# Performance work log

Hardware: AMD Instinct MI355X
Metric: run time of the kernel (lower is better)

The kernel has to match this reference:

```python
import jax, jax.numpy as jnp
import numpy as np

BOS, PAD, EOS, UNK = 0, 1, 2, 3  # fairseq dictionary special-token ids
CHAR_VOCAB = 5000
DIM = 512
LATENT = 10000


def setup_inputs() -> dict:
    key = jax.random.key(0)
    k1, k2, k3 = jax.random.split(key, 3)
    # char-ngram ids per token: [B, T, max_char_len]
    x = jax.random.randint(k1, (8, 1024, 20), 0, CHAR_VOCAB, dtype=jnp.int64 if jax.config.jax_enable_x64 else jnp.int32)
    # char ngram embedding table (also serves as preset_emb for special tokens)
    char_table = jax.random.normal(k2, (CHAR_VOCAB, DIM), dtype=jnp.float32) * 0.05
    # fixed latent codebook, init std = latent**-0.5 as in the module
    latent_mat = jax.random.normal(k3, (LATENT, DIM), dtype=jnp.float32) * (LATENT ** -0.5)
    return {"x": x, "char_table": char_table, "latent_mat": latent_mat}


def reference(x, char_table, latent_mat):
    # --- CharacterNgramEmbedder: gather + sum-pool over char ngrams (pad masked) ---
    emb = char_table[x]                                   # [B, T, C, D]
    valid = (x != PAD)[..., None].astype(emb.dtype)       # pad ngrams contribute 0
    ngram_weight = jnp.sum(emb * valid, axis=2)           # [B, T, D]
    lang_emb = jnp.tanh(ngram_weight)

    # --- latent codebook attention: QK^T -> softmax -> V over fixed codebook ---
    latent_scores = jnp.einsum('btd,ld->btl', lang_emb, latent_mat)   # [B, T, L]
    latent_dist = jax.nn.softmax(latent_scores, axis=-1)
    latent_emb = jnp.einsum('btl,ld->btd', latent_dist, latent_mat)   # [B, T, D]
    sde_emb = lang_emb + latent_emb

    # --- preset_emb overwrite for special tokens (masked scatter) ---
    first = x[:, :, 0]                                    # [B, T]
    for tok in (PAD, BOS, EOS, UNK):
        sde_emb = jnp.where((first == tok)[..., None], char_table[tok], sde_emb)
    return sde_emb
```

## Files before the change

### kernel.cpp

```cpp
#include <hip/hip_runtime.h>

#define BT    8192
#define DIM   512
#define NLAT  10000
#define LPAD2 10240
#define NG    20

typedef short bf16x8 __attribute__((ext_vector_type(8)));
typedef float f32x4  __attribute__((ext_vector_type(4)));
typedef unsigned short u16;
typedef u16 u16x8 __attribute__((ext_vector_type(8)));
typedef u16 u16x4 __attribute__((ext_vector_type(4)));

static __device__ __forceinline__ u16 f2bf(float f) {
    union { float f; unsigned u; } v; v.f = f;
    unsigned r = v.u + 0x7FFF + ((v.u >> 16) & 1);
    return (u16)(r >> 16);
}

static __device__ __forceinline__ void gload16(const void* g, void* l) {
    __builtin_amdgcn_global_load_lds(
        (const __attribute__((address_space(1))) unsigned int*)g,
        (__attribute__((address_space(3))) unsigned int*)l,
        16, 0, 0);
}

__global__ __launch_bounds__(256) void lang_kernel(
        const int* __restrict__ x, const float* __restrict__ ct,
        float* __restrict__ lang, u16* __restrict__ qb) {
    const int tok = blockIdx.x * 2 + (threadIdx.x >> 7);
    const int tl  = threadIdx.x & 127;
    const int* xr = x + tok * NG;
    float4 s = make_float4(0.f, 0.f, 0.f, 0.f);
    #pragma unroll
    for (int j = 0; j < NG; ++j) {
        int c = xr[j];
        if (c != 1) {
            float4 v = *(const float4*)(ct + (long)c * DIM + tl * 4);
            s.x += v.x; s.y += v.y; s.z += v.z; s.w += v.w;
        }
    }
    float4 t = make_float4(tanhf(s.x), tanhf(s.y), tanhf(s.z), tanhf(s.w));
    *(float4*)(lang + (long)tok * DIM + tl * 4) = t;
    u16x4 o = { f2bf(t.x), f2bf(t.y), f2bf(t.z), f2bf(t.w) };
    *(u16x4*)(qb + (long)tok * DIM + tl * 4) = o;
}

__global__ __launch_bounds__(256) void conv_kernel(
        const float* __restrict__ lm, u16* __restrict__ kvg, u16* __restrict__ latT) {
    __shared__ u16 tile[64][514];
    const int lb = blockIdx.x * 64;
    const int t  = threadIdx.x;

    #pragma unroll 4
    for (int i = 0; i < 16; ++i) {
        int ch  = t + i * 256;
        int r   = ch >> 6;
        int c8  = ch & 63;
        int row = lb + r;
        u16x8 v = {0,0,0,0,0,0,0,0};
        if (row < NLAT) {
            const float* src = lm + (long)row * DIM + c8 * 8;
            float4 a = *(const float4*)src;
            float4 b = *(const float4*)(src + 4);
            v[0]=f2bf(a.x); v[1]=f2bf(a.y); v[2]=f2bf(a.z); v[3]=f2bf(a.w);
            v[4]=f2bf(b.x); v[5]=f2bf(b.y); v[6]=f2bf(b.z); v[7]=f2bf(b.w);
        }
        *(u16x8*)(kvg + (long)row * DIM + c8 * 8) = v;
        #pragma unroll
        for (int j = 0; j < 8; ++j) tile[r][c8 * 8 + j] = v[j];
    }
    __syncthreads();
    #pragma unroll 4
    for (int i = 0; i < 16; ++i) {
        int ch = t + i * 256;
        int d  = ch >> 3;
        int c8 = ch & 7;
        u16x8 v;
        #pragma unroll
        for (int j = 0; j < 8; ++j) v[j] = tile[c8 * 8 + j][d];
        *(u16x8*)(latT + (long)d * LPAD2 + lb + c8 * 8) = v;
    }
}

#define G_COMPUTE(buf) {                                                       \
    _Pragma("unroll")                                                          \
    for (int kc_ = 0; kc_ < 2; ++kc_) {                                        \
        const int xs_ = ((kc_ * 4 + g) ^ (lr & 7)) * 8;                        \
        bf16x8 af_[2], bf_[4];                                                 \
        _Pragma("unroll")                                                      \
        for (int mf_ = 0; mf_ < 2; ++mf_)                                      \
            af_[mf_] = *(const bf16x8*)&lds[buf][(wm * 32 + mf_ * 16 + lr) * 64 + xs_]; \
        _Pragma("unroll")                                                      \
        for (int nf_ = 0; nf_ < 4; ++nf_)                                      \
            bf_[nf_] = *(const bf16x8*)&lds[buf][8192 + (wn * 64 + nf_ * 16 + lr) * 64 + xs_]; \
        __builtin_amdgcn_s_setprio(1);                                         \
        _Pragma("unroll")                                                      \
        for (int mf_ = 0; mf_ < 2; ++mf_)                                      \
            _Pragma("unroll")                                                  \
            for (int nf_ = 0; nf_ < 4; ++nf_)                                  \
                acc[mf_][nf_] = __builtin_amdgcn_mfma_f32_16x16x32_bf16(       \
                    af_[mf_], bf_[nf_], acc[mf_][nf_], 0, 0, 0);               \
        __builtin_amdgcn_s_setprio(0);                                         \
    }                                                                          \
}

#define G1_STAGE(buf, kt) {                                                    \
    const int k0_ = (kt) * 64;                                                 \
    _Pragma("unroll")                                                          \
    for (int i_ = 0; i_ < 2; ++i_) {                                           \
        int ch_ = t + i_ * 512;                                                \
        int row_ = ch_ >> 3;                                                   \
        int sc_ = ((ch_ & 7) ^ (row_ & 7)) * 8;                                \
        gload16(Q + (m0 + row_) * (long)DIM + k0_ + sc_, &lds[buf][ch_ * 8]);  \
        gload16(Bgp + (long)row_ * DIM + k0_ + sc_, &lds[buf][8192 + ch_ * 8]);\
    }                                                                          \
}

__global__ __launch_bounds__(512, 4) void gemm1_kernel(
        const u16* __restrict__ Q, const u16* __restrict__ L,
        u16* __restrict__ P, float* __restrict__ rowsum,
        int n0_global, int npanels, int pstride) {
    __shared__ u16 lds[2][16384];

    const int nwg = 64 * npanels;
    const int cpx = nwg >> 3;
    const int bid = blockIdx.x;
    const int wg  = (bid & 7) * cpx + (bid >> 3);
    const int mb  = wg & 63;
    const int nb  = wg >> 6;
    const long m0    = (long)mb * 128;
    const int  ncol0 = n0_global + nb * 128;

    const u16* Bgp = L + (long)ncol0 * DIM;

    const int t = threadIdx.x, lane = t & 63, w = t >> 6;
    const int wm = w >> 1, wn = w & 1;
    const int g = lane >> 4, lr = lane & 15;

    f32x4 acc[2][4];
    #pragma unroll
    for (int m = 0; m < 2; ++m)
        #pragma unroll
        for (int n = 0; n < 4; ++n) acc[m][n] = f32x4{0.f,0.f,0.f,0.f};

    G1_STAGE(0, 0);
    G1_STAGE(1, 1);

    #pragma unroll 1
    for (int kt = 0; kt < 7; ++kt) {
        asm volatile("s_waitcnt vmcnt(4)" ::: "memory");
        __builtin_amdgcn_s_barrier();
        G_COMPUTE(kt & 1);
        __builtin_amdgcn_s_barrier();
        if (kt + 2 < 8) G1_STAGE(kt & 1, kt + 2);
    }
    asm volatile("s_waitcnt vmcnt(0)" ::: "memory");
    __builtin_amdgcn_s_barrier();
    G_COMPUTE(1);

    #pragma unroll
    for (int mf = 0; mf < 2; ++mf)
        #pragma unroll
        for (int nf = 0; nf < 4; ++nf) {
            const int col = ncol0 + wn * 64 + nf * 16 + lr;
            const bool ok = (col < NLAT);
            #pragma unroll
            for (int r = 0; r < 4; ++r)
                acc[mf][nf][r] = ok ? __expf(acc[mf][nf][r]) : 0.f;
        }

    #pragma unroll
    for (int mf = 0; mf < 2; ++mf) {
        float sv[4] = {0.f, 0.f, 0.f, 0.f};
        #pragma unroll
        for (int nf = 0; nf < 4; ++nf)
            #pragma unroll
            for (int r = 0; r < 4; ++r) sv[r] += acc[mf][nf][r];
        #pragma unroll
        for (int r = 0; r < 4; ++r) {
            float s = sv[r];
            s += __shfl_xor(s, 1); s += __shfl_xor(s, 2);
            s += __shfl_xor(s, 4); s += __shfl_xor(s, 8);
            if (lr == 0)
                atomicAdd(&rowsum[m0 + wm * 32 + mf * 16 + g * 4 + r], s);
        }
    }

    const int pcol0 = (ncol0 - n0_global) + wn * 64;
    #pragma unroll
    for (int mf = 0; mf < 2; ++mf)
        #pragma unroll
        for (int nf = 0; nf < 4; ++nf) {
            const int pc = pcol0 + nf * 16 + lr;
            #pragma unroll
            for (int r = 0; r < 4; ++r) {
                const long row = m0 + wm * 32 + mf * 16 + g * 4 + r;
                __builtin_nontemporal_store(f2bf(acc[mf][nf][r]),
                                            &P[row * (long)pstride + pc]);
            }
        }
}

#define G2_STAGE(buf, kt) {                                                    \
    const int kloc_ = (step_off + (kt)) * 64;                                  \
    _Pragma("unroll")                                                          \
    for (int i_ = 0; i_ < 2; ++i_) {                                           \
        int ch_ = t + i_ * 512;                                                \
        int row_ = ch_ >> 3;                                                   \
        int sc_ = ((ch_ & 7) ^ (row_ & 7)) * 8;                                \
        gload16(P + (m0 + row_) * (long)pstride + kloc_ + sc_, &lds[buf][ch_ * 8]); \
        gload16(LT + (long)(nbase + row_) * LPAD2 + n0_global + kloc_ + sc_,   \
                &lds[buf][8192 + ch_ * 8]);                                    \
    }                                                                          \
}

__global__ __launch_bounds__(512, 4) void gemm2_kernel(
        const u16* __restrict__ P, const u16* __restrict__ LT,
        float* __restrict__ out, float* __restrict__ part0,
        int pstride, int kcols, int n0_global, int splitk, int accum) {
    __shared__ u16 lds[2][16384];

    const int nwg = 64 * 4 * splitk;
    const int cpx = nwg >> 3;
    const int bid = blockIdx.x;
    const int wg  = (bid & 7) * cpx + (bid >> 3);
    const int mb  = wg & 63;
    const int rest = wg >> 6;
    const int nb  = rest / splitk;
    const int s   = rest % splitk;

    const long m0    = (long)mb * 128;
    const int  nbase = nb * 128;

    const int nsteps = kcols / 64;
    const int q = nsteps / splitk, rr = nsteps % splitk;
    const int psteps   = q + (s < rr ? 1 : 0);
    const int step_off = s * q + (s < rr ? s : rr);

    const int t = threadIdx.x, lane = t & 63, w = t >> 6;
    const int wm = w >> 1, wn = w & 1;
    const int g = lane >> 4, lr = lane & 15;

    float* buf = (s == 0) ? out : part0;

    f32x4 acc[2][4];
    #pragma unroll
    for (int m = 0; m < 2; ++m)
        #pragma unroll
        for (int n = 0; n < 4; ++n) acc[m][n] = f32x4{0.f,0.f,0.f,0.f};

    G2_STAGE(0, 0);
    if (psteps > 1) G2_STAGE(1, 1);

    #pragma unroll 1
    for (int kt = 0; kt < psteps - 1; ++kt) {
        asm volatile("s_waitcnt vmcnt(4)" ::: "memory");
        __builtin_amdgcn_s_barrier();
        G_COMPUTE(kt & 1);
        __builtin_amdgcn_s_barrier();
        if (kt + 2 < psteps) G2_STAGE(kt & 1, kt + 2);
    }
    asm volatile("s_waitcnt vmcnt(0)" ::: "memory");
    __builtin_amdgcn_s_barrier();
    G_COMPUTE((psteps - 1) & 1);

    #pragma unroll
    for (int mf = 0; mf < 2; ++mf)
        #pragma unroll
        for (int nf = 0; nf < 4; ++nf) {
            const int col = nbase + wn * 64 + nf * 16 + lr;
            #pragma unroll
            for (int r = 0; r < 4; ++r) {
                const long row = m0 + wm * 32 + mf * 16 + g * 4 + r;
                float v = acc[mf][nf][r];
                if (accum) v += buf[row * DIM + col];
                buf[row * DIM + col] = v;
            }
        }
}

__global__ __launch_bounds__(256) void final_kernel(
        float* __restrict__ out, const float* __restrict__ part0,
        const float* __restrict__ lang, const float* __restrict__ rowsum,
        const int* __restrict__ x, const float* __restrict__ ct, int nparts) {
    const int tok   = blockIdx.x;
    const float inv = 1.f / rowsum[tok];
    const int first = x[tok * NG];
    #pragma unroll
    for (int i = 0; i < 2; ++i) {
        const int col = threadIdx.x + i * 256;
        float v = out[(long)tok * DIM + col];
        if (nparts > 1) v += part0[(long)tok * DIM + col];
        v = v * inv + lang[(long)tok * DIM + col];
        if (first < 4) v = ct[first * DIM + col];
        out[(long)tok * DIM + col] = v;
    }
}

extern "C" void kernel_launch(void* const* d_in, const int* in_sizes, int n_in,
                              void* d_out, int out_size, void* d_ws, size_t ws_size,
                              hipStream_t stream) {
    const int*   x  = (const int*)d_in[0];
    const float* ct = (const float*)d_in[1];
    const float* lm = (const float*)d_in[2];
    float* out = (float*)d_out;

    char* ws = (char*)d_ws;
    size_t off = 0;
    u16*   qb   = (u16*)(ws + off);   off += (size_t)BT * DIM * 2;
    float* lang = (float*)(ws + off); off += (size_t)BT * DIM * 4;
    u16*   kvg  = (u16*)(ws + off);   off += (size_t)LPAD2 * DIM * 2;
    u16*   latT = (u16*)(ws + off);   off += (size_t)DIM * LPAD2 * 2;
    float* rowsum = (float*)(ws + off); off += (size_t)BT * 4;
    u16*   P    = (u16*)(ws + off);
    const size_t fixed = off;

    const int panels_total = LPAD2 / 128;
    const size_t pfull = (size_t)BT * LPAD2 * 2;
    const size_t partb = (size_t)BT * DIM * 4;

    int splitk = 1, ppc = panels_total;
    float* part0 = out;
    if (ws_size >= fixed + pfull + partb) {
        splitk = 2;
        part0 = (float*)(ws + fixed + pfull);
    } else if (ws_size >= fixed + pfull) {
        splitk = 1;
    } else {
        size_t avail = (ws_size > fixed) ? (ws_size - fixed) : 0;
        size_t p = avail / ((size_t)BT * 128 * 2);
        ppc = (int)(p < 1 ? 1 : (p > (size_t)panels_total ? (size_t)panels_total : p));
    }
    const int pstride = ppc * 128;

    hipMemsetAsync(rowsum, 0, (size_t)BT * 4, stream);
    lang_kernel<<<BT / 2, 256, 0, stream>>>(x, ct, lang, qb);
    conv_kernel<<<LPAD2 / 64, 256, 0, stream>>>(lm, kvg, latT);

    int chunk = 0;
    for (int cs = 0; cs < panels_total; cs += ppc, ++chunk) {
        const int np = (panels_total - cs < ppc) ? (panels_total - cs) : ppc;
        gemm1_kernel<<<64 * np, 512, 0, stream>>>(qb, kvg, P, rowsum,
                                                  cs * 128, np, pstride);
        gemm2_kernel<<<64 * 4 * splitk, 512, 0, stream>>>(P, latT, out, part0,
                                                          pstride, np * 128, cs * 128,
                                                          splitk, chunk > 0 ? 1 : 0);
    }
    final_kernel<<<BT, 256, 0, stream>>>(out, part0, lang, rowsum, x, ct, splitk);
}
```

Before: 337.8 us.

## Gather bf16 char table in lang kernel and stage P stores through LDS

Adds a kernel that converts the char embedding table to bf16, so the ngram gather-sum reads half the bytes and each thread handles 8 elements. gemm1 now writes its exp'd probabilities into a swizzled LDS tile and then issues coalesced 16-byte stores of P, replacing scattered 2-byte nontemporal stores. This adds an extra kernel launch and an LDS barrier. The ngram sums also lose precision because the table is rounded to bf16 before summing.

```diff
diff --git a/kernel.cpp b/kernel.cpp
--- a/kernel.cpp
+++ b/kernel.cpp
@@ -5,6 +5,7 @@
 #define NLAT  10000
 #define LPAD2 10240
 #define NG    20
+#define CV    5000
 
 typedef short bf16x8 __attribute__((ext_vector_type(8)));
 typedef float f32x4  __attribute__((ext_vector_type(4)));
@@ -17,6 +18,9 @@
     unsigned r = v.u + 0x7FFF + ((v.u >> 16) & 1);
     return (u16)(r >> 16);
 }
+static __device__ __forceinline__ float bf2f(u16 b) {
+    union { unsigned u; float f; } v; v.u = ((unsigned)b) << 16; return v.f;
+}
 
 static __device__ __forceinline__ void gload16(const void* g, void* l) {
     __builtin_amdgcn_global_load_lds(
@@ -25,25 +29,42 @@
         16, 0, 0);
 }
 
+__global__ __launch_bounds__(256) void ct2bf_kernel(
+        const float* __restrict__ ct, u16* __restrict__ ctb) {
+    const long base = ((long)blockIdx.x * 256 + threadIdx.x) * 8;
+    float4 a = *(const float4*)(ct + base);
+    float4 b = *(const float4*)(ct + base + 4);
+    u16x8 v = { f2bf(a.x), f2bf(a.y), f2bf(a.z), f2bf(a.w),
+                f2bf(b.x), f2bf(b.y), f2bf(b.z), f2bf(b.w) };
+    *(u16x8*)(ctb + base) = v;
+}
+
 __global__ __launch_bounds__(256) void lang_kernel(
-        const int* __restrict__ x, const float* __restrict__ ct,
+        const int* __restrict__ x, const u16* __restrict__ ctb,
         float* __restrict__ lang, u16* __restrict__ qb) {
-    const int tok = blockIdx.x * 2 + (threadIdx.x >> 7);
-    const int tl  = threadIdx.x & 127;
+    const int tok = blockIdx.x * 4 + (threadIdx.x >> 6);
+    const int tl  = threadIdx.x & 63;
     const int* xr = x + tok * NG;
-    float4 s = make_float4(0.f, 0.f, 0.f, 0.f);
+    float s[8];
+    #pragma unroll
+    for (int i = 0; i < 8; ++i) s[i] = 0.f;
     #pragma unroll
     for (int j = 0; j < NG; ++j) {
         int c = xr[j];
         if (c != 1) {
-            float4 v = *(const float4*)(ct + (long)c * DIM + tl * 4);
-            s.x += v.x; s.y += v.y; s.z += v.z; s.w += v.w;
-        }
-    }
-    float4 t = make_float4(tanhf(s.x), tanhf(s.y), tanhf(s.z), tanhf(s.w));
-    *(float4*)(lang + (long)tok * DIM + tl * 4) = t;
-    u16x4 o = { f2bf(t.x), f2bf(t.y), f2bf(t.z), f2bf(t.w) };
-    *(u16x4*)(qb + (long)tok * DIM + tl * 4) = o;
+            u16x8 v = *(const u16x8*)(ctb + (long)c * DIM + tl * 8);
+            #pragma unroll
+            for (int i = 0; i < 8; ++i) s[i] += bf2f(v[i]);
+        }
+    }
+    float4 lo, hi;
+    lo.x = tanhf(s[0]); lo.y = tanhf(s[1]); lo.z = tanhf(s[2]); lo.w = tanhf(s[3]);
+    hi.x = tanhf(s[4]); hi.y = tanhf(s[5]); hi.z = tanhf(s[6]); hi.w = tanhf(s[7]);
+    *(float4*)(lang + (long)tok * DIM + tl * 8)     = lo;
+    *(float4*)(lang + (long)tok * DIM + tl * 8 + 4) = hi;
+    u16x8 o = { f2bf(lo.x), f2bf(lo.y), f2bf(lo.z), f2bf(lo.w),
+                f2bf(hi.x), f2bf(hi.y), f2bf(hi.z), f2bf(hi.w) };
+    *(u16x8*)(qb + (long)tok * DIM + tl * 8) = o;
 }
 
 __global__ __launch_bounds__(256) void conv_kernel(
@@ -165,9 +186,14 @@
         for (int nf = 0; nf < 4; ++nf) {
             const int col = ncol0 + wn * 64 + nf * 16 + lr;
             const bool ok = (col < NLAT);
+            const int lcol = wn * 64 + nf * 16 + lr;
             #pragma unroll
-            for (int r = 0; r < 4; ++r)
-                acc[mf][nf][r] = ok ? __expf(acc[mf][nf][r]) : 0.f;
+            for (int r = 0; r < 4; ++r) {
+                float p = ok ? __expf(acc[mf][nf][r]) : 0.f;
+                acc[mf][nf][r] = p;
+                const int row = wm * 32 + mf * 16 + g * 4 + r;
+                lds[0][row * 128 + (lcol ^ ((row & 15) << 3))] = f2bf(p);
+            }
         }
 
     #pragma unroll
@@ -187,19 +213,15 @@
         }
     }
 
-    const int pcol0 = (ncol0 - n0_global) + wn * 64;
-    #pragma unroll
-    for (int mf = 0; mf < 2; ++mf)
-        #pragma unroll
-        for (int nf = 0; nf < 4; ++nf) {
-            const int pc = pcol0 + nf * 16 + lr;
-            #pragma unroll
-            for (int r = 0; r < 4; ++r) {
-                const long row = m0 + wm * 32 + mf * 16 + g * 4 + r;
-                __builtin_nontemporal_store(f2bf(acc[mf][nf][r]),
-                                            &P[row * (long)pstride + pc]);
-            }
-        }
+    __syncthreads();
+    const int pbase = ncol0 - n0_global;
+    #pragma unroll
+    for (int it = 0; it < 4; ++it) {
+        const int flat = t + it * 512;
+        const int row = flat >> 4, ck = flat & 15;
+        u16x8 v = *(const u16x8*)&lds[0][row * 128 + ((ck ^ (row & 15)) * 8)];
+        *(u16x8*)(P + (m0 + row) * (long)pstride + pbase + ck * 8) = v;
+    }
 }
 
 #define G2_STAGE(buf, kt) {                                                    \
@@ -312,6 +334,7 @@
     float* lang = (float*)(ws + off); off += (size_t)BT * DIM * 4;
     u16*   kvg  = (u16*)(ws + off);   off += (size_t)LPAD2 * DIM * 2;
     u16*   latT = (u16*)(ws + off);   off += (size_t)DIM * LPAD2 * 2;
+    u16*   ctb  = (u16*)(ws + off);   off += (size_t)CV * DIM * 2;
     float* rowsum = (float*)(ws + off); off += (size_t)BT * 4;
     u16*   P    = (u16*)(ws + off);
     const size_t fixed = off;
@@ -335,7 +358,8 @@
     const int pstride = ppc * 128;
 
     hipMemsetAsync(rowsum, 0, (size_t)BT * 4, stream);
-    lang_kernel<<<BT / 2, 256, 0, stream>>>(x, ct, lang, qb);
+    ct2bf_kernel<<<CV * DIM / (256 * 8), 256, 0, stream>>>(ct, ctb);
+    lang_kernel<<<BT / 4, 256, 0, stream>>>(x, ctb, lang, qb);
     conv_kernel<<<LPAD2 / 64, 256, 0, stream>>>(lm, kvg, latT);
 
     int chunk = 0;
```

After: 294.7 us. 1.15x faster.
